# Performance work log

Measured on AMD Instinct MI355X. Metric: run time of the kernel, lower is better.

## Reference

```python
import jax, jax.numpy as jnp
import numpy as np

N_HEAD = 16
N_FEAT = 1024
HEAD_DIM = N_FEAT // N_HEAD


def setup_inputs() -> dict:
    key = jax.random.key(0)
    ks = jax.random.split(key, 13)
    B, Tq, Tc = 2, 1024, 1024
    s = 0.02
    return {
        "query": jax.random.normal(ks[0], (B, Tq, N_FEAT), jnp.float32),
        "key": jax.random.normal(ks[1], (B, Tq, N_FEAT), jnp.float32),
        "value": jax.random.normal(ks[2], (B, Tq, N_FEAT), jnp.float32),
        "cache": jax.random.normal(ks[3], (B, N_HEAD, Tc, 2 * HEAD_DIM), jnp.float32),
        "Wq": jax.random.normal(ks[4], (N_FEAT, N_FEAT), jnp.float32) * s,
        "bq": jax.random.normal(ks[5], (N_FEAT,), jnp.float32) * s,
        "Wk": jax.random.normal(ks[6], (N_FEAT, N_FEAT), jnp.float32) * s,
        "bk": jax.random.normal(ks[7], (N_FEAT,), jnp.float32) * s,
        "Wv": jax.random.normal(ks[8], (N_FEAT, N_FEAT), jnp.float32) * s,
        "bv": jax.random.normal(ks[9], (N_FEAT,), jnp.float32) * s,
        "Wo": jax.random.normal(ks[10], (N_FEAT, N_FEAT), jnp.float32) * s,
        "bo": jax.random.normal(ks[11], (N_FEAT,), jnp.float32) * s,
    }


def _split_heads(x, B):
    # [B, T, C] -> [B, H, T, D]
    return x.reshape(B, -1, N_HEAD, HEAD_DIM).transpose(0, 2, 1, 3)


def reference(query, key, value, cache, Wq, bq, Wk, bk, Wv, bv, Wo, bo):
    B, Tq, _ = query.shape
    # torch Linear: y = x @ W.T + b
    q = _split_heads(query @ Wq.T + bq, B)   # [B,H,Tq,D]
    k = _split_heads(key @ Wk.T + bk, B)     # [B,H,Tk,D]
    v = _split_heads(value @ Wv.T + bv, B)
    # KV-cache concat (cache holds [K | V] along last dim)
    k_cache, v_cache = jnp.split(cache, 2, axis=-1)
    k = jnp.concatenate([k_cache, k], axis=2)
    v = jnp.concatenate([v_cache, v], axis=2)
    new_cache = jnp.concatenate([k, v], axis=-1)
    scores = jnp.einsum("bhqd,bhkd->bhqk", q, k) / np.sqrt(HEAD_DIM).astype(jnp.float32)
    attn = jax.nn.softmax(scores, axis=-1)  # fake mask path; dropout is identity (rate 0 / eval)
    x = jnp.einsum("bhqk,bhkd->bhqd", attn, v)
    x = x.transpose(0, 2, 1, 3).reshape(B, Tq, N_FEAT)
    out = x @ Wo.T + bo
    return out, new_cache
```

## Files before the change

### kernel.cpp

```cpp
#include <hip/hip_runtime.h>

typedef short short4s __attribute__((ext_vector_type(4)));
typedef short short8 __attribute__((ext_vector_type(8)));
typedef __bf16 bf16x8 __attribute__((ext_vector_type(8)));
typedef float f32x4 __attribute__((ext_vector_type(4)));

#define NFEAT 1024
#define HDIM  64
#define NHEAD 16
#define TC2   2048
#define QSCL  0.18033688011112043f

__device__ __forceinline__ short f2bf(float f) {
    unsigned int u = __builtin_bit_cast(unsigned int, f);
    u += 0x7fffu + ((u >> 16) & 1u);
    return (short)(u >> 16);
}
__device__ __forceinline__ short f2bfq(float f) {
    __bf16 h = (__bf16)f;
    return __builtin_bit_cast(short, h);
}
__device__ __forceinline__ float bf2f(short s) {
    unsigned int u = ((unsigned int)(unsigned short)s) << 16;
    return __builtin_bit_cast(float, u);
}

__device__ __forceinline__ f32x4 mfma_bf16(short8 a, short8 b, f32x4 c) {
    return __builtin_amdgcn_mfma_f32_16x16x32_bf16(
        __builtin_bit_cast(bf16x8, a), __builtin_bit_cast(bf16x8, b), c, 0, 0, 0);
}

#define GLOAD16(gp, lp) __builtin_amdgcn_global_load_lds( \
    (const __attribute__((address_space(1))) void*)(gp),  \
    (__attribute__((address_space(3))) void*)(lp), 16, 0, 0)

__global__ __launch_bounds__(256) void prep_kernel(
    const float* __restrict__ q, const float* __restrict__ k, const float* __restrict__ v,
    const float* __restrict__ Wq, const float* __restrict__ Wk,
    const float* __restrict__ Wv, const float* __restrict__ Wo,
    const float4* __restrict__ cache4,
    short* __restrict__ qin, short* __restrict__ kin, short* __restrict__ vin,
    short* __restrict__ wqb, short* __restrict__ wkb, short* __restrict__ wvb,
    short* __restrict__ wob,
    float4* __restrict__ nc4, short* __restrict__ kbb, short* __restrict__ vtb)
{
    __shared__ short Vt[64 * 72];
    const int b = blockIdx.x, tid = threadIdx.x;
    if (b < 1280) {
        const float* src; short* dst; size_t base;
        if (b < 256)        { src = q;  dst = qin; base = (size_t)b * 8192; }
        else if (b < 512)   { src = k;  dst = kin; base = (size_t)(b - 256) * 8192; }
        else if (b < 768)   { src = v;  dst = vin; base = (size_t)(b - 512) * 8192; }
        else if (b < 896)   { src = Wq; dst = wqb; base = (size_t)(b - 768) * 8192; }
        else if (b < 1024)  { src = Wk; dst = wkb; base = (size_t)(b - 896) * 8192; }
        else if (b < 1152)  { src = Wv; dst = wvb; base = (size_t)(b - 1024) * 8192; }
        else                { src = Wo; dst = wob; base = (size_t)(b - 1152) * 8192; }
        const size_t off = base + (size_t)tid * 8;
        float4 a[8];
#pragma unroll
        for (int s = 0; s < 4; ++s) {
            a[2*s]   = *(const float4*)(src + off + s * 2048);
            a[2*s+1] = *(const float4*)(src + off + s * 2048 + 4);
        }
#pragma unroll
        for (int s = 0; s < 4; ++s) {
            short8 o;
            o[0] = f2bf(a[2*s].x);   o[1] = f2bf(a[2*s].y);
            o[2] = f2bf(a[2*s].z);   o[3] = f2bf(a[2*s].w);
            o[4] = f2bf(a[2*s+1].x); o[5] = f2bf(a[2*s+1].y);
            o[6] = f2bf(a[2*s+1].z); o[7] = f2bf(a[2*s+1].w);
            *(short8*)(dst + off + s * 2048) = o;
        }
    } else {
        const int cb = b - 1280;
        const int bh = cb >> 4, t0 = (cb & 15) * 64;
        const int col4 = tid & 31, r0 = tid >> 5;
        const float4* src = cache4 + ((size_t)bh * 1024 + t0 + r0) * 32 + col4;
        float4* ncr = nc4 + ((size_t)bh * TC2 + t0 + r0) * 32 + col4;
        float4 a[8];
#pragma unroll
        for (int j = 0; j < 8; ++j) a[j] = src[j * 256];
#pragma unroll
        for (int j = 0; j < 8; ++j) ncr[j * 256] = a[j];
        if (col4 < 16) {
#pragma unroll
            for (int j = 0; j < 8; ++j) {
                short4s kp;
                kp[0] = f2bf(a[j].x); kp[1] = f2bf(a[j].y);
                kp[2] = f2bf(a[j].z); kp[3] = f2bf(a[j].w);
                *(short4s*)&kbb[((size_t)bh * TC2 + t0 + r0 + 8 * j) * 64 + col4 * 4] = kp;
            }
        } else {
            const int d = (col4 - 16) * 4;
#pragma unroll
            for (int j = 0; j < 8; ++j) {
                int r = r0 + 8 * j;
                Vt[(d + 0) * 72 + r] = f2bf(a[j].x);
                Vt[(d + 1) * 72 + r] = f2bf(a[j].y);
                Vt[(d + 2) * 72 + r] = f2bf(a[j].z);
                Vt[(d + 3) * 72 + r] = f2bf(a[j].w);
            }
        }
        __syncthreads();
        const int d = tid >> 2, seg = (tid & 3) * 16;
        short* vd = &vtb[((size_t)bh * HDIM + d) * TC2 + t0 + seg];
        *(short8*)(vd)     = *(const short8*)&Vt[d * 72 + seg];
        *(short8*)(vd + 8) = *(const short8*)&Vt[d * 72 + seg + 8];
    }
}

__global__ __launch_bounds__(256) void gemm64(
    const short* __restrict__ A0, const short* __restrict__ A1, const short* __restrict__ A2,
    const short* __restrict__ W0, const short* __restrict__ W1, const short* __restrict__ W2,
    const float* __restrict__ b0, const float* __restrict__ b1, const float* __restrict__ b2,
    float* __restrict__ outf, short* __restrict__ qbuf, short* __restrict__ kbb,
    short* __restrict__ vtbp, int base_mode)
{
    __shared__ short As[64 * 64];
    __shared__ short Bs[128 * 64];

    const int orig = (blockIdx.z * gridDim.y + blockIdx.y) * gridDim.x + blockIdx.x;
    const int chunk = (gridDim.x * gridDim.y * gridDim.z) >> 3;
    const int newid = (orig & 7) * chunk + (orig >> 3);
    const int rem = newid & 255;
    const int by = rem >> 3, bx = rem & 7;

    int mode;
    const short *A, *W;
    const float* bias;
    if (base_mode == 3) { mode = 3; A = A0; W = W0; bias = b0; }
    else {
        mode = newid >> 8;
        if (mode == 0)      { A = A0; W = W0; bias = b0; }
        else if (mode == 1) { A = A1; W = W1; bias = b1; }
        else                { A = A2; W = W2; bias = b2; }
    }

    const int tid = threadIdx.x, lane = tid & 63, w = tid >> 6;
    const int lr = lane & 15, lg = lane >> 4;

    f32x4 acc[4][2];
#pragma unroll
    for (int m = 0; m < 4; ++m)
#pragma unroll
        for (int n = 0; n < 2; ++n) acc[m][n] = (f32x4){0.f, 0.f, 0.f, 0.f};

    const short* agBase = A + (size_t)(by * 64 + w * 16 + (lane >> 3)) * 1024 + (lane & 7) * 8;
    const short* bgBase = W + (size_t)(bx * 128 + w * 32 + (lane >> 3)) * 1024 + (lane & 7) * 8;
    short* asW = &As[w * 1024];
    short* bsW = &Bs[w * 2048];

    for (int kt = 0; kt < 16; ++kt) {
        const short* ag = agBase + kt * 64;
        const short* bg = bgBase + kt * 64;
        GLOAD16(ag,          asW);
        GLOAD16(ag + 8192,   asW + 512);
        GLOAD16(bg,          bsW);
        GLOAD16(bg + 8192,   bsW + 512);
        GLOAD16(bg + 16384,  bsW + 1024);
        GLOAD16(bg + 24576,  bsW + 1536);
        __syncthreads();
#pragma unroll
        for (int kk = 0; kk < 2; ++kk) {
            short8 af[4], bf[2];
#pragma unroll
            for (int m = 0; m < 4; ++m)
                af[m] = *(const short8*)&As[(m * 16 + lr) * 64 + kk * 32 + lg * 8];
#pragma unroll
            for (int n = 0; n < 2; ++n)
                bf[n] = *(const short8*)&Bs[(w * 32 + n * 16 + lr) * 64 + kk * 32 + lg * 8];
#pragma unroll
            for (int m = 0; m < 4; ++m)
#pragma unroll
                for (int n = 0; n < 2; ++n)
                    acc[m][n] = mfma_bf16(af[m], bf[n], acc[m][n]);
        }
        __syncthreads();
    }

#pragma unroll
    for (int m = 0; m < 4; ++m) {
#pragma unroll
        for (int n = 0; n < 2; ++n) {
            const int cg = bx * 128 + w * 32 + n * 16 + lr;
            const int rg0 = by * 64 + m * 16 + lg * 4;
            const float bv = bias[cg];
            if (mode == 3) {
#pragma unroll
                for (int r = 0; r < 4; ++r)
                    outf[(size_t)(rg0 + r) * NFEAT + cg] = acc[m][n][r] + bv;
            } else {
                const int b = rg0 >> 10, t0 = rg0 & 1023;
                const int h = cg >> 6, d = cg & 63;
                const size_t bh = (size_t)b * NHEAD + h;
                if (mode == 0) {
#pragma unroll
                    for (int r = 0; r < 4; ++r)
                        qbuf[(bh * 1024 + t0 + r) * HDIM + d] = f2bf((acc[m][n][r] + bv) * QSCL);
                } else if (mode == 1) {
#pragma unroll
                    for (int r = 0; r < 4; ++r) {
                        float val = acc[m][n][r] + bv;
                        outf[(bh * TC2 + 1024 + t0 + r) * 128 + d] = val;
                        kbb[(bh * TC2 + 1024 + t0 + r) * HDIM + d] = f2bf(val);
                    }
                } else {
                    short4s pk;
#pragma unroll
                    for (int r = 0; r < 4; ++r) {
                        float val = acc[m][n][r] + bv;
                        outf[(bh * TC2 + 1024 + t0 + r) * 128 + 64 + d] = val;
                        pk[r] = f2bf(val);
                    }
                    *(short4s*)&vtbp[(bh * HDIM + d) * TC2 + 1024 + t0] = pk;
                }
            }
        }
    }
}

__global__ __launch_bounds__(512) void attn_kernel(
    const short* __restrict__ qb, const short* __restrict__ kb,
    const short* __restrict__ vtb, short* __restrict__ opart, float* __restrict__ lbuf)
{
    __shared__ short Ks[2][64 * 64];
    __shared__ short Vs[2][64 * 64];
    __shared__ short Ps[8][16 * 32];

    const int tid = threadIdx.x, lane = tid & 63, w = tid >> 6;
    const int lr = lane & 15, lg = lane >> 4;
    const int b0 = blockIdx.x;
    const int xcd = b0 & 7, rest = b0 >> 3;
    const int unit = xcd + 8 * (rest & 15);
    const int qt = rest >> 4;
    const int bh = unit >> 2, quarter = unit & 3;
    const int xz = lr & 7;

    const short* qrow = qb + ((size_t)bh * 1024 + qt * 128 + w * 16 + lr) * HDIM + lg * 8;
    const short8 bq0 = *(const short8*)(qrow);
    const short8 bq1 = *(const short8*)(qrow + 32);

    const int srow = tid >> 3;
    const int scx = ((tid & 7) ^ (srow & 7)) * 8;
    const short* kgb = kb  + ((size_t)bh * TC2 + quarter * 512 + srow) * HDIM + scx;
    const short* vgb = vtb + ((size_t)bh * HDIM + srow) * TC2 + quarter * 512 + scx;
    short* kdst = &Ks[0][0] + w * 512;
    short* vdst = &Vs[0][0] + w * 512;

#define STAGE(bufsel, kvt_) do {                                         \
        const short* kg_ = kgb + (size_t)(kvt_) * 64 * HDIM;             \
        const short* vg_ = vgb + (kvt_) * 64;                            \
        GLOAD16(kg_, kdst + (bufsel) * 4096);                            \
        GLOAD16(vg_, vdst + (bufsel) * 4096);                            \
    } while (0)

    f32x4 accx[4];
#pragma unroll
    for (int i = 0; i < 4; ++i) accx[i] = (f32x4){0.f, 0.f, 0.f, 0.f};
    float lsp = 0.f;
    short* pw = &Ps[w][0];

    STAGE(0, 0);
    __syncthreads();

    int cur = 0;
    for (int kvt = 0; kvt < 8; ++kvt) {
        if (kvt < 7) STAGE(cur ^ 1, kvt + 1);
        const short* Kc = &Ks[cur][0];
        const short* Vc = &Vs[cur][0];

        f32x4 s[4];
#pragma unroll
        for (int n = 0; n < 4; ++n) {
            const short* kt = Kc + (n * 16 + lr) * 64;
            short8 k0 = *(const short8*)&kt[(lg ^ xz) * 8];
            short8 k1 = *(const short8*)&kt[((4 + lg) ^ xz) * 8];
            s[n] = (f32x4){0.f, 0.f, 0.f, 0.f};
            s[n] = mfma_bf16(k0, bq0, s[n]);
            s[n] = mfma_bf16(k1, bq1, s[n]);
        }

        float p[4][4];
#pragma unroll
        for (int n = 0; n < 4; ++n)
#pragma unroll
            for (int r = 0; r < 4; ++r) p[n][r] = __builtin_amdgcn_exp2f(s[n][r]);
        float sm[8];
#pragma unroll
        for (int i = 0; i < 8; ++i) sm[i] = p[i >> 1][(i & 1) * 2] + p[i >> 1][(i & 1) * 2 + 1];
        lsp += ((sm[0] + sm[1]) + (sm[2] + sm[3])) + ((sm[4] + sm[5]) + (sm[6] + sm[7]));

#pragma unroll
        for (int ks = 0; ks < 2; ++ks) {
            __builtin_amdgcn_sched_barrier(0);
#pragma unroll
            for (int np = 0; np < 2; ++np) {
                int n = 2 * ks + np;
                short4s pk;
                pk[0] = f2bfq(p[n][0]); pk[1] = f2bfq(p[n][1]);
                pk[2] = f2bfq(p[n][2]); pk[3] = f2bfq(p[n][3]);
                int slot = (2 * np + (lg >> 1)) ^ (lr & 3);
                *(short4s*)&pw[lr * 32 + slot * 8 + (lg & 1) * 4] = pk;
            }
            short8 ap = *(const short8*)&pw[lr * 32 + (lg ^ (lr & 3)) * 8];
#pragma unroll
            for (int nd = 0; nd < 4; ++nd) {
                const short* vt = Vc + (nd * 16 + lr) * 64;
                short8 vf = *(const short8*)&vt[((ks * 4 + lg) ^ xz) * 8];
                accx[nd] = mfma_bf16(ap, vf, accx[nd]);
            }
        }

        __syncthreads();
        cur ^= 1;
    }

    float ls = lsp;
    ls += __shfl_xor(ls, 16);
    ls += __shfl_xor(ls, 32);
    const size_t rbase = (size_t)quarter * 32768 + (size_t)bh * 1024 + qt * 128 + w * 16;
#pragma unroll
    for (int nd = 0; nd < 4; ++nd)
#pragma unroll
        for (int r = 0; r < 4; ++r)
            opart[(rbase + lg * 4 + r) * 64 + nd * 16 + lr] = f2bfq(accx[nd][r]);
    if (lg == 0) lbuf[rbase + lr] = ls;
#undef STAGE
}

__global__ __launch_bounds__(256) void combine_kernel(
    const short* __restrict__ opart, const float* __restrict__ lbuf,
    short* __restrict__ xb)
{
    int idx = blockIdx.x * 256 + threadIdx.x;
    int r = idx >> 3, d8 = (idx & 7) * 8;
    float l = lbuf[r] + lbuf[32768 + r] + lbuf[65536 + r] + lbuf[98304 + r];
    float acc[8];
#pragma unroll
    for (int j = 0; j < 8; ++j) acc[j] = 0.f;
#pragma unroll
    for (int i = 0; i < 4; ++i) {
        short8 op = *(const short8*)&opart[((size_t)i * 32768 + r) * 64 + d8];
#pragma unroll
        for (int j = 0; j < 8; ++j) acc[j] += bf2f(op[j]);
    }
    float inv = 1.0f / l;
    short8 o;
#pragma unroll
    for (int j = 0; j < 8; ++j) o[j] = f2bfq(acc[j] * inv);
    int bh = r >> 10, tq = r & 1023;
    int b = bh >> 4, h = bh & 15;
    *(short8*)&xb[((size_t)(b * 1024 + tq)) * NFEAT + h * 64 + d8] = o;
}

extern "C" void kernel_launch(void* const* d_in, const int* in_sizes, int n_in,
                              void* d_out, int out_size, void* d_ws, size_t ws_size,
                              hipStream_t stream) {
    const float* query = (const float*)d_in[0];
    const float* key   = (const float*)d_in[1];
    const float* value = (const float*)d_in[2];
    const float* cache = (const float*)d_in[3];
    const float* Wq = (const float*)d_in[4];
    const float* bq = (const float*)d_in[5];
    const float* Wk = (const float*)d_in[6];
    const float* bk = (const float*)d_in[7];
    const float* Wv = (const float*)d_in[8];
    const float* bv = (const float*)d_in[9];
    const float* Wo = (const float*)d_in[10];
    const float* bo = (const float*)d_in[11];

    float* out0   = (float*)d_out;
    float* ncache = out0 + (size_t)2 * 1024 * 1024;

    short* qin = (short*)d_ws;
    short* kin = qin + (size_t)2097152;
    short* vin = kin + (size_t)2097152;
    short* wqb = vin + (size_t)2097152;
    short* wkb = wqb + (size_t)1048576;
    short* wvb = wkb + (size_t)1048576;
    short* wob = wvb + (size_t)1048576;
    short* qbuf = wob + (size_t)1048576;
    short* kbb  = qbuf + (size_t)2097152;
    short* vtb  = kbb  + (size_t)4194304;
    short* opart = (short*)d_ws;
    float* lbuf  = (float*)(qin + (size_t)8388608);
    short* xb    = qbuf;

    prep_kernel<<<1792, 256, 0, stream>>>(query, key, value, Wq, Wk, Wv, Wo,
        (const float4*)cache, qin, kin, vin, wqb, wkb, wvb, wob,
        (float4*)ncache, kbb, vtb);

    gemm64<<<dim3(8, 32, 3), 256, 0, stream>>>(qin, kin, vin, wqb, wkb, wvb,
        bq, bk, bv, ncache, qbuf, kbb, vtb, 0);

    attn_kernel<<<1024, 512, 0, stream>>>(qbuf, kbb, vtb, opart, lbuf);

    combine_kernel<<<1024, 256, 0, stream>>>(opart, lbuf, xb);

    gemm64<<<dim3(8, 32, 1), 256, 0, stream>>>(xb, nullptr, nullptr, wob, nullptr, nullptr,
        bo, nullptr, nullptr, out0, nullptr, nullptr, nullptr, 3);
}
```

Baseline: 99.62 us.

## Process two query tiles per attention block to reuse staged K/V

Each attention block now handles 256 query rows (two 128-row sub-tiles per wave) instead of 128, so each K/V tile staged into shared memory feeds twice as many MFMAs. The grid is halved to 512 blocks and launch bounds request 4 blocks per CU. This aims to cut global-to-LDS K/V traffic and staging overhead per query. The cost is more registers for the extra accumulators and Q fragments, and fewer blocks to spread across the CUs.

```diff
diff --git a/kernel.cpp b/kernel.cpp
--- a/kernel.cpp
+++ b/kernel.cpp
@@ -219,7 +219,7 @@
     }
 }
 
-__global__ __launch_bounds__(512) void attn_kernel(
+__global__ __launch_bounds__(512, 4) void attn_kernel(
     const short* __restrict__ qb, const short* __restrict__ kb,
     const short* __restrict__ vtb, short* __restrict__ opart, float* __restrict__ lbuf)
 {
@@ -236,9 +236,12 @@
     const int bh = unit >> 2, quarter = unit & 3;
     const int xz = lr & 7;
 
-    const short* qrow = qb + ((size_t)bh * 1024 + qt * 128 + w * 16 + lr) * HDIM + lg * 8;
-    const short8 bq0 = *(const short8*)(qrow);
-    const short8 bq1 = *(const short8*)(qrow + 32);
+    const short* qrow0 = qb + ((size_t)bh * 1024 + qt * 256 + w * 16 + lr) * HDIM + lg * 8;
+    const short* qrow1 = qrow0 + (size_t)128 * HDIM;
+    const short8 bq00 = *(const short8*)(qrow0);
+    const short8 bq01 = *(const short8*)(qrow0 + 32);
+    const short8 bq10 = *(const short8*)(qrow1);
+    const short8 bq11 = *(const short8*)(qrow1 + 32);
 
     const int srow = tid >> 3;
     const int scx = ((tid & 7) ^ (srow & 7)) * 8;
@@ -254,10 +257,13 @@
         GLOAD16(vg_, vdst + (bufsel) * 4096);                            \
     } while (0)
 
-    f32x4 accx[4];
-#pragma unroll
-    for (int i = 0; i < 4; ++i) accx[i] = (f32x4){0.f, 0.f, 0.f, 0.f};
-    float lsp = 0.f;
+    f32x4 acc0[4], acc1[4];
+#pragma unroll
+    for (int i = 0; i < 4; ++i) {
+        acc0[i] = (f32x4){0.f, 0.f, 0.f, 0.f};
+        acc1[i] = (f32x4){0.f, 0.f, 0.f, 0.f};
+    }
+    float lsp0 = 0.f, lsp1 = 0.f;
     short* pw = &Ps[w][0];
 
     STAGE(0, 0);
@@ -269,45 +275,53 @@
         const short* Kc = &Ks[cur][0];
         const short* Vc = &Vs[cur][0];
 
-        f32x4 s[4];
-#pragma unroll
-        for (int n = 0; n < 4; ++n) {
-            const short* kt = Kc + (n * 16 + lr) * 64;
-            short8 k0 = *(const short8*)&kt[(lg ^ xz) * 8];
-            short8 k1 = *(const short8*)&kt[((4 + lg) ^ xz) * 8];
-            s[n] = (f32x4){0.f, 0.f, 0.f, 0.f};
-            s[n] = mfma_bf16(k0, bq0, s[n]);
-            s[n] = mfma_bf16(k1, bq1, s[n]);
-        }
-
-        float p[4][4];
-#pragma unroll
-        for (int n = 0; n < 4; ++n)
-#pragma unroll
-            for (int r = 0; r < 4; ++r) p[n][r] = __builtin_amdgcn_exp2f(s[n][r]);
-        float sm[8];
-#pragma unroll
-        for (int i = 0; i < 8; ++i) sm[i] = p[i >> 1][(i & 1) * 2] + p[i >> 1][(i & 1) * 2 + 1];
-        lsp += ((sm[0] + sm[1]) + (sm[2] + sm[3])) + ((sm[4] + sm[5]) + (sm[6] + sm[7]));
-
-#pragma unroll
-        for (int ks = 0; ks < 2; ++ks) {
-            __builtin_amdgcn_sched_barrier(0);
-#pragma unroll
-            for (int np = 0; np < 2; ++np) {
-                int n = 2 * ks + np;
-                short4s pk;
-                pk[0] = f2bfq(p[n][0]); pk[1] = f2bfq(p[n][1]);
-                pk[2] = f2bfq(p[n][2]); pk[3] = f2bfq(p[n][3]);
-                int slot = (2 * np + (lg >> 1)) ^ (lr & 3);
-                *(short4s*)&pw[lr * 32 + slot * 8 + (lg & 1) * 4] = pk;
+#pragma unroll
+        for (int mblk = 0; mblk < 2; ++mblk) {
+            const short8 bq0 = mblk ? bq10 : bq00;
+            const short8 bq1 = mblk ? bq11 : bq01;
+            f32x4* accx = mblk ? acc1 : acc0;
+
+            f32x4 s[4];
+#pragma unroll
+            for (int n = 0; n < 4; ++n) {
+                const short* kt = Kc + (n * 16 + lr) * 64;
+                short8 k0 = *(const short8*)&kt[(lg ^ xz) * 8];
+                short8 k1 = *(const short8*)&kt[((4 + lg) ^ xz) * 8];
+                s[n] = (f32x4){0.f, 0.f, 0.f, 0.f};
+                s[n] = mfma_bf16(k0, bq0, s[n]);
+                s[n] = mfma_bf16(k1, bq1, s[n]);
             }
-            short8 ap = *(const short8*)&pw[lr * 32 + (lg ^ (lr & 3)) * 8];
-#pragma unroll
-            for (int nd = 0; nd < 4; ++nd) {
-                const short* vt = Vc + (nd * 16 + lr) * 64;
-                short8 vf = *(const short8*)&vt[((ks * 4 + lg) ^ xz) * 8];
-                accx[nd] = mfma_bf16(ap, vf, accx[nd]);
+
+            float p[4][4];
+#pragma unroll
+            for (int n = 0; n < 4; ++n)
+#pragma unroll
+                for (int r = 0; r < 4; ++r) p[n][r] = __builtin_amdgcn_exp2f(s[n][r]);
+            float sm[8];
+#pragma unroll
+            for (int i = 0; i < 8; ++i) sm[i] = p[i >> 1][(i & 1) * 2] + p[i >> 1][(i & 1) * 2 + 1];
+            float rs = ((sm[0] + sm[1]) + (sm[2] + sm[3])) + ((sm[4] + sm[5]) + (sm[6] + sm[7]));
+            if (mblk) lsp1 += rs; else lsp0 += rs;
+
+#pragma unroll
+            for (int ks = 0; ks < 2; ++ks) {
+                __builtin_amdgcn_sched_barrier(0);
+#pragma unroll
+                for (int np = 0; np < 2; ++np) {
+                    int n = 2 * ks + np;
+                    short4s pk;
+                    pk[0] = f2bfq(p[n][0]); pk[1] = f2bfq(p[n][1]);
+                    pk[2] = f2bfq(p[n][2]); pk[3] = f2bfq(p[n][3]);
+                    int slot = (2 * np + (lg >> 1)) ^ (lr & 3);
+                    *(short4s*)&pw[lr * 32 + slot * 8 + (lg & 1) * 4] = pk;
+                }
+                short8 ap = *(const short8*)&pw[lr * 32 + (lg ^ (lr & 3)) * 8];
+#pragma unroll
+                for (int nd = 0; nd < 4; ++nd) {
+                    const short* vt = Vc + (nd * 16 + lr) * 64;
+                    short8 vf = *(const short8*)&vt[((ks * 4 + lg) ^ xz) * 8];
+                    accx[nd] = mfma_bf16(ap, vf, accx[nd]);
+                }
             }
         }
 
@@ -315,16 +329,21 @@
         cur ^= 1;
     }
 
-    float ls = lsp;
-    ls += __shfl_xor(ls, 16);
-    ls += __shfl_xor(ls, 32);
-    const size_t rbase = (size_t)quarter * 32768 + (size_t)bh * 1024 + qt * 128 + w * 16;
-#pragma unroll
-    for (int nd = 0; nd < 4; ++nd)
-#pragma unroll
-        for (int r = 0; r < 4; ++r)
-            opart[(rbase + lg * 4 + r) * 64 + nd * 16 + lr] = f2bfq(accx[nd][r]);
-    if (lg == 0) lbuf[rbase + lr] = ls;
+#pragma unroll
+    for (int mblk = 0; mblk < 2; ++mblk) {
+        float ls = mblk ? lsp1 : lsp0;
+        ls += __shfl_xor(ls, 16);
+        ls += __shfl_xor(ls, 32);
+        const f32x4* accx = mblk ? acc1 : acc0;
+        const size_t rbase = (size_t)quarter * 32768 + (size_t)bh * 1024
+                           + qt * 256 + mblk * 128 + w * 16;
+#pragma unroll
+        for (int nd = 0; nd < 4; ++nd)
+#pragma unroll
+            for (int r = 0; r < 4; ++r)
+                opart[(rbase + lg * 4 + r) * 64 + nd * 16 + lr] = f2bfq(accx[nd][r]);
+        if (lg == 0) lbuf[rbase + lr] = ls;
+    }
 #undef STAGE
 }
 
@@ -393,7 +412,7 @@
     gemm64<<<dim3(8, 32, 3), 256, 0, stream>>>(qin, kin, vin, wqb, wkb, wvb,
         bq, bk, bv, ncache, qbuf, kbb, vtb, 0);
 
-    attn_kernel<<<1024, 512, 0, stream>>>(qbuf, kbb, vtb, opart, lbuf);
+    attn_kernel<<<512, 512, 0, stream>>>(qbuf, kbb, vtb, opart, lbuf);
 
     combine_kernel<<<1024, 256, 0, stream>>>(opart, lbuf, xb);
 
```

After: 101.6 us. 2.0% more time.
